# Optimization experiments

Measured on AMD Instinct MI355X. Metric: run time of the kernel, lower is better.

## Reference

```python
import jax, jax.numpy as jnp
import numpy as np

NEG = -1e9

def setup_inputs() -> dict:
    key = jax.random.key(0)
    ks = jax.random.split(key, 6)
    B, T, H = 32, 2048, 1024
    dec = jax.random.normal(ks[0], (B, H), dtype=jnp.float32)
    enc = jax.random.normal(ks[1], (B, T, H), dtype=jnp.float32)
    mask = jax.random.randint(ks[2], (B, T), 0, 2).astype(jnp.int32)
    scale = 1.0 / np.sqrt(H)
    W_enc = jax.random.normal(ks[3], (H, H), dtype=jnp.float32) * scale
    W_dec = jax.random.normal(ks[4], (H, H), dtype=jnp.float32) * scale
    v = jax.random.normal(ks[5], (H,), dtype=jnp.float32) * scale
    return {"decoder_hidden": dec, "encoder_outputs": enc, "mask": mask,
            "W_enc": W_enc, "W_dec": W_dec, "v": v}

def reference(decoder_hidden, encoder_outputs, mask, W_enc, W_dec, v):
    # enc proj: [B,T,H] @ W_enc^T ; dec proj: [B,H] @ W_dec^T broadcast over T
    enc_p = jnp.einsum('bth,oh->bto', encoder_outputs, W_enc)
    dec_p = jnp.einsum('bh,oh->bo', decoder_hidden, W_dec)[:, None, :]  # [B,1,H]
    energy = jnp.tanh(enc_p + dec_p)                                    # [B,T,H]
    scores = jnp.einsum('bth,h->bt', energy, v)                         # [B,T]
    scores = jnp.where(mask == 0, NEG, scores)
    attn_weights = jax.nn.softmax(scores, axis=1)                       # [B,T]
    context = jnp.einsum('bt,bth->bh', attn_weights, encoder_outputs)   # [B,H]
    return (context, attn_weights)
```

## Files before the change

### kernel.cpp

```cpp
#include <hip/hip_runtime.h>
#include <hip/hip_bf16.h>
#include <stdint.h>

#define B_ 32
#define T_ 2048
#define H_ 1024
#define M_ (B_*T_)

typedef __bf16 bf16x8 __attribute__((ext_vector_type(8)));
typedef float  f32x4  __attribute__((ext_vector_type(4)));
typedef float  f32x16 __attribute__((ext_vector_type(16)));

__device__ __forceinline__ float tanh_fast(float x) {
    float e = __expf(2.0f * x);
    return 1.0f - 2.0f / (e + 1.0f);
}

__device__ __forceinline__ bf16x8 cvt2(f32x4 f0, f32x4 f1) {
    bf16x8 h;
    h[0] = (__bf16)f0[0]; h[1] = (__bf16)f0[1]; h[2] = (__bf16)f0[2]; h[3] = (__bf16)f0[3];
    h[4] = (__bf16)f1[0]; h[5] = (__bf16)f1[1]; h[6] = (__bf16)f1[2]; h[7] = (__bf16)f1[3];
    return h;
}

__global__ __launch_bounds__(256) void k_prep(const float* __restrict__ We,
                                              __bf16* __restrict__ Wt,
                                              const float* __restrict__ dec,
                                              const float* __restrict__ Wd,
                                              float* __restrict__ decp) {
    int bx = blockIdx.x;
    int tid = threadIdx.x;
    if (bx < 512) {
        int tg = bx * 256 + tid;
        int lane = tg & 63;
        int c = (tg >> 6) & 31;
        int s = tg >> 11;
        int o = c * 32 + (lane & 31);
        int k = s * 16 + (lane >> 5) * 8;
        const f32x4* src = (const f32x4*)&We[(size_t)o * H_ + k];
        *(bf16x8*)&Wt[(size_t)tg * 8] = cvt2(src[0], src[1]);
    } else {
        int bxd = bx - 512;
        int b = bxd & 31, oc = bxd >> 5;
        int o = oc * 64 + (tid >> 2);
        int kq = tid & 3;
        const f32x4* wr = (const f32x4*)&Wd[(size_t)o * H_ + kq * 256];
        const f32x4* dr = (const f32x4*)&dec[(size_t)b * H_ + kq * 256];
        f32x4 s4 = {0.f, 0.f, 0.f, 0.f};
#pragma unroll 8
        for (int i = 0; i < 64; ++i) s4 += wr[i] * dr[i];
        float s = s4[0] + s4[1] + s4[2] + s4[3];
        s += __shfl_xor(s, 1);
        s += __shfl_xor(s, 2);
        if (kq == 0) decp[b * H_ + o] = s;
    }
}

__global__ __launch_bounds__(256, 2) void k_scores(const float* __restrict__ enc,
                                                   const float* __restrict__ decp,
                                                   const __bf16* __restrict__ Wt,
                                                   const float* __restrict__ v,
                                                   float* __restrict__ scores_p) {
    __shared__ __bf16 A_lds[2][64 * 32 * 8];
    __shared__ float red[4][64];

    const int tid = threadIdx.x;
    const int w = tid >> 6, lane = tid & 63;
    const int l5 = lane & 31, q2 = lane >> 5;

    const int bx = blockIdx.x;
    const int xs = bx & 7;
    const int q = bx >> 3;
    const int nt = q & 3;
    const int rg = (q >> 2) * 8 + xs;
    const int m0 = rg * 64;
    const int b = m0 >> 11;
    const int cg0 = nt * 8 + w * 2;

    float dp[2], vvv[2];
#pragma unroll
    for (int ct = 0; ct < 2; ++ct) {
        int col = (cg0 + ct) * 32 + l5;
        dp[ct]  = decp[b * H_ + col];
        vvv[ct] = v[col];
    }

    f32x16 acc[2][2];
#pragma unroll
    for (int rt = 0; rt < 2; ++rt)
#pragma unroll
        for (int ct = 0; ct < 2; ++ct)
#pragma unroll
            for (int g = 0; g < 16; ++g)
                acc[rt][ct][g] = dp[ct];

    const int ko_s = tid & 31;
    const int rbase = (tid >> 5) * 8;
    const float* sbase = &enc[(size_t)(m0 + rbase) * H_ + ko_s * 8];

    {
#pragma unroll
        for (int i = 0; i < 8; ++i) {
            const f32x4* s4 = (const f32x4*)(sbase + (size_t)i * H_);
            int row = rbase + i;
            int cell = row * 32 + ((ko_s & 24) | ((ko_s ^ row) & 7));
            *(bf16x8*)&A_lds[0][cell * 8] = cvt2(s4[0], s4[1]);
        }
    }
    __syncthreads();

    bf16x8 bb[4][2];
#pragma unroll
    for (int p = 0; p < 4; ++p)
#pragma unroll
        for (int ct = 0; ct < 2; ++ct)
            bb[p][ct] = *(const bf16x8*)&Wt[(((size_t)p * 32 + cg0 + ct) * 64 + lane) * 8];

#pragma unroll 1
    for (int kc = 0; kc < 4; ++kc) {
        const __bf16* buf = A_lds[kc & 1];

        f32x4 sr[8][2];
        if (kc < 3) {
            const float* sp0 = sbase + (size_t)(kc + 1) * 256;
#pragma unroll
            for (int i = 0; i < 8; ++i) {
                const f32x4* s4 = (const f32x4*)(sp0 + (size_t)i * H_);
                sr[i][0] = s4[0];
                sr[i][1] = s4[1];
            }
        }

        bf16x8 af[2][2];
#pragma unroll
        for (int p = 0; p < 2; ++p)
#pragma unroll
            for (int rt = 0; rt < 2; ++rt) {
                int row = rt * 32 + l5;
                int ko = p * 2 + q2;
                int cell = row * 32 + ((ko & 24) | ((ko ^ row) & 7));
                af[p][rt] = *(const bf16x8*)&buf[cell * 8];
            }

#pragma unroll
        for (int sl = 0; sl < 16; ++sl) {
            const int s = kc * 16 + sl;
            bf16x8 a0 = af[sl & 1][0], a1 = af[sl & 1][1];
            bf16x8 w0 = bb[s & 3][0],  w1 = bb[s & 3][1];

            {
                int sn = (s + 4) & 63;
#pragma unroll
                for (int ct = 0; ct < 2; ++ct)
                    bb[s & 3][ct] = *(const bf16x8*)&Wt[(((size_t)sn * 32 + cg0 + ct) * 64 + lane) * 8];
            }
            {
                int sl2 = (sl + 2) & 15;
#pragma unroll
                for (int rt = 0; rt < 2; ++rt) {
                    int row = rt * 32 + l5;
                    int ko = sl2 * 2 + q2;
                    int cell = row * 32 + ((ko & 24) | ((ko ^ row) & 7));
                    af[sl & 1][rt] = *(const bf16x8*)&buf[cell * 8];
                }
            }

            acc[0][0] = __builtin_amdgcn_mfma_f32_32x32x16_bf16(a0, w0, acc[0][0], 0, 0, 0);
            acc[0][1] = __builtin_amdgcn_mfma_f32_32x32x16_bf16(a0, w1, acc[0][1], 0, 0, 0);
            acc[1][0] = __builtin_amdgcn_mfma_f32_32x32x16_bf16(a1, w0, acc[1][0], 0, 0, 0);
            acc[1][1] = __builtin_amdgcn_mfma_f32_32x32x16_bf16(a1, w1, acc[1][1], 0, 0, 0);
        }

        if (kc < 3) {
            __bf16* dst = A_lds[(kc + 1) & 1];
#pragma unroll
            for (int i = 0; i < 8; ++i) {
                int row = rbase + i;
                int cell = row * 32 + ((ko_s & 24) | ((ko_s ^ row) & 7));
                *(bf16x8*)&dst[cell * 8] = cvt2(sr[i][0], sr[i][1]);
            }
        }
        __syncthreads();
    }

    float sp[2][16];
#pragma unroll
    for (int rt = 0; rt < 2; ++rt)
#pragma unroll
        for (int g = 0; g < 16; ++g)
            sp[rt][g] = tanh_fast(acc[rt][0][g]) * vvv[0] + tanh_fast(acc[rt][1][g]) * vvv[1];

#pragma unroll
    for (int rt = 0; rt < 2; ++rt)
#pragma unroll
        for (int g = 0; g < 16; ++g) {
            float s = sp[rt][g];
            s += __shfl_xor(s, 1);
            s += __shfl_xor(s, 2);
            s += __shfl_xor(s, 4);
            s += __shfl_xor(s, 8);
            s += __shfl_xor(s, 16);
            sp[rt][g] = s;
        }

    if (l5 == 0) {
#pragma unroll
        for (int rt = 0; rt < 2; ++rt)
#pragma unroll
            for (int g = 0; g < 16; ++g) {
                int row = rt * 32 + (g & 3) + 8 * (g >> 2) + 4 * q2;
                red[w][row] = sp[rt][g];
            }
    }
    __syncthreads();
    if (tid < 64) {
        float s = red[0][tid] + red[1][tid] + red[2][tid] + red[3][tid];
        scores_p[nt * M_ + m0 + tid] = s;
    }
}

__global__ __launch_bounds__(256) void k_softmax(const float* __restrict__ scores_p,
                                                 const int* __restrict__ mask,
                                                 float* __restrict__ attn) {
    int b = blockIdx.x;
    int tid = threadIdx.x;
    int w = tid >> 6, lane = tid & 63;
    __shared__ float sm[2][4];
    float val[8];
    float mx = -3e38f;
#pragma unroll
    for (int ii = 0; ii < 8; ++ii) {
        int idx = b * T_ + tid + ii * 256;
        float s = scores_p[idx] + scores_p[M_ + idx] + scores_p[2 * M_ + idx] + scores_p[3 * M_ + idx];
        s = (mask[idx] == 0) ? -1e9f : s;
        val[ii] = s;
        mx = fmaxf(mx, s);
    }
#pragma unroll
    for (int m = 1; m <= 32; m <<= 1) mx = fmaxf(mx, __shfl_xor(mx, m));
    if (lane == 0) sm[0][w] = mx;
    __syncthreads();
    mx = fmaxf(fmaxf(sm[0][0], sm[0][1]), fmaxf(sm[0][2], sm[0][3]));
    float lsum = 0.f;
#pragma unroll
    for (int ii = 0; ii < 8; ++ii) {
        val[ii] = __expf(val[ii] - mx);
        lsum += val[ii];
    }
#pragma unroll
    for (int m = 1; m <= 32; m <<= 1) lsum += __shfl_xor(lsum, m);
    if (lane == 0) sm[1][w] = lsum;
    __syncthreads();
    float inv = 1.0f / (sm[1][0] + sm[1][1] + sm[1][2] + sm[1][3]);
#pragma unroll
    for (int ii = 0; ii < 8; ++ii)
        attn[b * T_ + tid + ii * 256] = val[ii] * inv;
}

__global__ __launch_bounds__(512) void k_context(const float* __restrict__ enc,
                                                 const float* __restrict__ attn,
                                                 float* __restrict__ ctx) {
    __shared__ f32x4 cred[8][32];
    int bx = blockIdx.x;
    int b = bx >> 3, hc = bx & 7;
    int tid = threadIdx.x;
    int wv = tid >> 6, lane = tid & 63;
    int l5 = lane & 31, tq2 = lane >> 5;
    int h = hc * 128 + l5 * 4;
    const float* ap = &attn[b * T_ + wv * 256 + tq2];
    const float* ep = &enc[((size_t)b * T_ + wv * 256 + tq2) * H_ + h];
    f32x4 acc = {0.f, 0.f, 0.f, 0.f};
#pragma unroll 8
    for (int i = 0; i < 128; ++i) {
        float a = ap[2 * i];
        f32x4 e = *(const f32x4*)(ep + (size_t)2 * i * H_);
        acc += a * e;
    }
#pragma unroll
    for (int c = 0; c < 4; ++c) acc[c] += __shfl_xor(acc[c], 32);
    if (tq2 == 0) cred[wv][l5] = acc;
    __syncthreads();
    if (tid < 32) {
        f32x4 r = cred[0][tid];
#pragma unroll
        for (int j = 1; j < 8; ++j) r += cred[j][tid];
        *(f32x4*)&ctx[b * H_ + hc * 128 + tid * 4] = r;
    }
}

extern "C" void kernel_launch(void* const* d_in, const int* in_sizes, int n_in,
                              void* d_out, int out_size, void* d_ws, size_t ws_size,
                              hipStream_t stream) {
    (void)in_sizes; (void)n_in; (void)out_size; (void)ws_size;
    const float* dec  = (const float*)d_in[0];
    const float* enc  = (const float*)d_in[1];
    const int*   mask = (const int*)d_in[2];
    const float* We   = (const float*)d_in[3];
    const float* Wd   = (const float*)d_in[4];
    const float* v    = (const float*)d_in[5];

    float* out = (float*)d_out;
    char* ws = (char*)d_ws;
    float*  decp     = (float*)ws;
    float*  scores_p = (float*)(ws + 131072);
    __bf16* Wt       = (__bf16*)(ws + 131072 + 1048576);

    k_prep   <<<1024, 256, 0, stream>>>(We, Wt, dec, Wd, decp);
    k_scores <<<4096, 256, 0, stream>>>(enc, decp, Wt, v, scores_p);
    k_softmax<<<32, 256, 0, stream>>>(scores_p, mask, out + B_ * H_);
    k_context<<<256, 512, 0, stream>>>(enc, out + B_ * H_, out);
}
```

Baseline: 582.1 us.

## Pre-convert encoder to bf16 fragment layout and DMA it into LDS for scores GEMM

Adds a separate pass that converts the fp32 encoder outputs into a bf16 copy laid out in MFMA fragment order in workspace. The scores GEMM then streams that copy into LDS with global_load_lds DMA, using 128-row tiles and 8 waves per block. This removes the in-loop fp32-to-bf16 conversion and swizzled LDS stores from the GEMM, and doubles row reuse of the weight fragments. In exchange it adds an extra full read of the encoder plus a 128MB write and reread, and it needs a large workspace, falling back to the old kernel otherwise.

```diff
diff --git a/kernel.cpp b/kernel.cpp
--- a/kernel.cpp
+++ b/kernel.cpp
@@ -21,6 +21,12 @@
     h[0] = (__bf16)f0[0]; h[1] = (__bf16)f0[1]; h[2] = (__bf16)f0[2]; h[3] = (__bf16)f0[3];
     h[4] = (__bf16)f1[0]; h[5] = (__bf16)f1[1]; h[6] = (__bf16)f1[2]; h[7] = (__bf16)f1[3];
     return h;
+}
+
+__device__ __forceinline__ void dma16(const void* g, void* l) {
+    __builtin_amdgcn_global_load_lds(
+        (const __attribute__((address_space(1))) unsigned int*)g,
+        (__attribute__((address_space(3))) unsigned int*)l, 16, 0, 0);
 }
 
 __global__ __launch_bounds__(256) void k_prep(const float* __restrict__ We,
@@ -56,18 +62,170 @@
     }
 }
 
-__global__ __launch_bounds__(256, 2) void k_scores(const float* __restrict__ enc,
+__global__ __launch_bounds__(256) void k_conv(const float* __restrict__ enc,
+                                              __bf16* __restrict__ encT) {
+    __shared__ float Lf[128][132];
+    const int rg = blockIdx.x;
+    const int t = threadIdx.x;
+    const size_t rowbase = (size_t)rg * 128;
+#pragma unroll 1
+    for (int kc = 0; kc < 8; ++kc) {
+#pragma unroll
+        for (int i = 0; i < 16; ++i) {
+            int row = i * 8 + (t >> 5);
+            int qq = t & 31;
+            f32x4 val = *(const f32x4*)&enc[(rowbase + row) * H_ + kc * 128 + qq * 4];
+            *(f32x4*)&Lf[row][qq * 4] = val;
+        }
+        __syncthreads();
+#pragma unroll
+        for (int j = 0; j < 8; ++j) {
+            int cid = j * 256 + t;
+            int g = cid >> 6;
+            int lane = cid & 63;
+            int rt = g & 3, s = g >> 2;
+            int row = rt * 32 + (lane & 31);
+            int kl = s * 16 + (lane >> 5) * 8;
+            f32x4 f0 = *(const f32x4*)&Lf[row][kl];
+            f32x4 f1 = *(const f32x4*)&Lf[row][kl + 4];
+            *(bf16x8*)&encT[((((size_t)rg * 8 + kc) * 32 + g) * 64 + lane) * 8] = cvt2(f0, f1);
+        }
+        __syncthreads();
+    }
+}
+
+__global__ __launch_bounds__(512, 4) void k_scores(const __bf16* __restrict__ encT,
                                                    const float* __restrict__ decp,
                                                    const __bf16* __restrict__ Wt,
                                                    const float* __restrict__ v,
                                                    float* __restrict__ scores_p) {
-    __shared__ __bf16 A_lds[2][64 * 32 * 8];
-    __shared__ float red[4][64];
+    __shared__ __align__(16) __bf16 Abuf[2][32 * 64 * 8];
+    __shared__ float red[4][128];
 
     const int tid = threadIdx.x;
     const int w = tid >> 6, lane = tid & 63;
     const int l5 = lane & 31, q2 = lane >> 5;
-
+    const int wr = w >> 2, wc = w & 3;
+
+    const int bx = blockIdx.x;
+    const int xs = bx & 7;
+    const int q = bx >> 3;
+    const int ng = q & 3;
+    const int rg = (q >> 2) * 8 + xs;
+    const int m0 = rg * 128;
+    const int b = m0 >> 11;
+    const int c0 = ng * 8 + wc * 2;
+
+    f32x16 acc[2][2];
+#pragma unroll
+    for (int ct = 0; ct < 2; ++ct) {
+        float dpv = decp[b * H_ + (c0 + ct) * 32 + l5];
+#pragma unroll
+        for (int rr = 0; rr < 2; ++rr)
+#pragma unroll
+            for (int g = 0; g < 16; ++g)
+                acc[rr][ct][g] = dpv;
+    }
+
+    const size_t chunk0 = ((size_t)rg * 8) * 32 * 512;
+
+#pragma unroll
+    for (int i = 0; i < 4; ++i) {
+        int g = w * 4 + i;
+        dma16(&encT[chunk0 + (size_t)g * 512 + lane * 8], &Abuf[0][g * 512]);
+    }
+    __syncthreads();
+
+    bf16x8 b_cur[2], b_nxt[2];
+#pragma unroll
+    for (int ct = 0; ct < 2; ++ct)
+        b_cur[ct] = *(const bf16x8*)&Wt[(((size_t)0 * 32 + c0 + ct) * 64 + lane) * 8];
+
+#pragma unroll 1
+    for (int kc = 0; kc < 8; ++kc) {
+        if (kc < 7) {
+            const size_t cb = ((size_t)(rg * 8 + kc + 1)) * 32 * 512;
+#pragma unroll
+            for (int i = 0; i < 4; ++i) {
+                int g = w * 4 + i;
+                dma16(&encT[cb + (size_t)g * 512 + lane * 8], &Abuf[(kc + 1) & 1][g * 512]);
+            }
+        }
+        const __bf16* buf = Abuf[kc & 1];
+
+#pragma unroll
+        for (int sl = 0; sl < 8; ++sl) {
+            int sgn = (kc * 8 + sl + 1) & 63;
+#pragma unroll
+            for (int ct = 0; ct < 2; ++ct)
+                b_nxt[ct] = *(const bf16x8*)&Wt[(((size_t)sgn * 32 + c0 + ct) * 64 + lane) * 8];
+
+            bf16x8 af[2];
+#pragma unroll
+            for (int rr = 0; rr < 2; ++rr)
+                af[rr] = *(const bf16x8*)&buf[((sl * 4 + wr * 2 + rr) * 64 + lane) * 8];
+
+            acc[0][0] = __builtin_amdgcn_mfma_f32_32x32x16_bf16(af[0], b_cur[0], acc[0][0], 0, 0, 0);
+            acc[0][1] = __builtin_amdgcn_mfma_f32_32x32x16_bf16(af[0], b_cur[1], acc[0][1], 0, 0, 0);
+            acc[1][0] = __builtin_amdgcn_mfma_f32_32x32x16_bf16(af[1], b_cur[0], acc[1][0], 0, 0, 0);
+            acc[1][1] = __builtin_amdgcn_mfma_f32_32x32x16_bf16(af[1], b_cur[1], acc[1][1], 0, 0, 0);
+
+            b_cur[0] = b_nxt[0];
+            b_cur[1] = b_nxt[1];
+        }
+        __syncthreads();
+    }
+
+    float vv[2];
+#pragma unroll
+    for (int ct = 0; ct < 2; ++ct) vv[ct] = v[(c0 + ct) * 32 + l5];
+
+    float sp[2][16];
+#pragma unroll
+    for (int rr = 0; rr < 2; ++rr)
+#pragma unroll
+        for (int g = 0; g < 16; ++g)
+            sp[rr][g] = tanh_fast(acc[rr][0][g]) * vv[0] + tanh_fast(acc[rr][1][g]) * vv[1];
+
+#pragma unroll
+    for (int rr = 0; rr < 2; ++rr)
+#pragma unroll
+        for (int g = 0; g < 16; ++g) {
+            float s = sp[rr][g];
+            s += __shfl_xor(s, 1);
+            s += __shfl_xor(s, 2);
+            s += __shfl_xor(s, 4);
+            s += __shfl_xor(s, 8);
+            s += __shfl_xor(s, 16);
+            sp[rr][g] = s;
+        }
+
+    if (l5 == 0) {
+#pragma unroll
+        for (int rr = 0; rr < 2; ++rr)
+#pragma unroll
+            for (int g = 0; g < 16; ++g) {
+                int row = wr * 64 + rr * 32 + (g & 3) + 8 * (g >> 2) + 4 * q2;
+                red[wc][row] = sp[rr][g];
+            }
+    }
+    __syncthreads();
+    if (tid < 128) {
+        float s = red[0][tid] + red[1][tid] + red[2][tid] + red[3][tid];
+        scores_p[ng * M_ + m0 + tid] = s;
+    }
+}
+
+__global__ __launch_bounds__(256, 2) void k_scores_fb(const float* __restrict__ enc,
+                                                      const float* __restrict__ decp,
+                                                      const __bf16* __restrict__ Wt,
+                                                      const float* __restrict__ v,
+                                                      float* __restrict__ scores_p) {
+    __shared__ __bf16 A_lds[2][64 * 32 * 8];
+    __shared__ float red[4][64];
+    const int tid = threadIdx.x;
+    const int w = tid >> 6, lane = tid & 63;
+    const int l5 = lane & 31, q2 = lane >> 5;
     const int bx = blockIdx.x;
     const int xs = bx & 7;
     const int q = bx >> 3;
@@ -76,28 +234,23 @@
     const int m0 = rg * 64;
     const int b = m0 >> 11;
     const int cg0 = nt * 8 + w * 2;
-
     float dp[2], vvv[2];
 #pragma unroll
     for (int ct = 0; ct < 2; ++ct) {
         int col = (cg0 + ct) * 32 + l5;
-        dp[ct]  = decp[b * H_ + col];
+        dp[ct] = decp[b * H_ + col];
         vvv[ct] = v[col];
     }
-
     f32x16 acc[2][2];
 #pragma unroll
     for (int rt = 0; rt < 2; ++rt)
 #pragma unroll
         for (int ct = 0; ct < 2; ++ct)
 #pragma unroll
-            for (int g = 0; g < 16; ++g)
-                acc[rt][ct][g] = dp[ct];
-
+            for (int g = 0; g < 16; ++g) acc[rt][ct][g] = dp[ct];
     const int ko_s = tid & 31;
     const int rbase = (tid >> 5) * 8;
     const float* sbase = &enc[(size_t)(m0 + rbase) * H_ + ko_s * 8];
-
     {
 #pragma unroll
         for (int i = 0; i < 8; ++i) {
@@ -108,88 +261,55 @@
         }
     }
     __syncthreads();
-
-    bf16x8 bb[4][2];
-#pragma unroll
-    for (int p = 0; p < 4; ++p)
-#pragma unroll
-        for (int ct = 0; ct < 2; ++ct)
-            bb[p][ct] = *(const bf16x8*)&Wt[(((size_t)p * 32 + cg0 + ct) * 64 + lane) * 8];
-
+    bf16x8 b_cur[2];
+#pragma unroll
+    for (int ct = 0; ct < 2; ++ct)
+        b_cur[ct] = *(const bf16x8*)&Wt[(((size_t)0 * 32 + cg0 + ct) * 64 + lane) * 8];
 #pragma unroll 1
     for (int kc = 0; kc < 4; ++kc) {
         const __bf16* buf = A_lds[kc & 1];
-
-        f32x4 sr[8][2];
+#pragma unroll
+        for (int sl = 0; sl < 16; ++sl) {
+            const int s = kc * 16 + sl;
+            int sn = (s + 1) & 63;
+            bf16x8 b_nxt[2];
+#pragma unroll
+            for (int ct = 0; ct < 2; ++ct)
+                b_nxt[ct] = *(const bf16x8*)&Wt[(((size_t)sn * 32 + cg0 + ct) * 64 + lane) * 8];
+            bf16x8 af[2];
+#pragma unroll
+            for (int rt = 0; rt < 2; ++rt) {
+                int row = rt * 32 + l5;
+                int ko = sl * 2 + q2;
+                int cell = row * 32 + ((ko & 24) | ((ko ^ row) & 7));
+                af[rt] = *(const bf16x8*)&buf[cell * 8];
+            }
+            acc[0][0] = __builtin_amdgcn_mfma_f32_32x32x16_bf16(af[0], b_cur[0], acc[0][0], 0, 0, 0);
+            acc[0][1] = __builtin_amdgcn_mfma_f32_32x32x16_bf16(af[0], b_cur[1], acc[0][1], 0, 0, 0);
+            acc[1][0] = __builtin_amdgcn_mfma_f32_32x32x16_bf16(af[1], b_cur[0], acc[1][0], 0, 0, 0);
+            acc[1][1] = __builtin_amdgcn_mfma_f32_32x32x16_bf16(af[1], b_cur[1], acc[1][1], 0, 0, 0);
+            b_cur[0] = b_nxt[0];
+            b_cur[1] = b_nxt[1];
+        }
         if (kc < 3) {
+            __bf16* dst = A_lds[(kc + 1) & 1];
             const float* sp0 = sbase + (size_t)(kc + 1) * 256;
 #pragma unroll
             for (int i = 0; i < 8; ++i) {
                 const f32x4* s4 = (const f32x4*)(sp0 + (size_t)i * H_);
-                sr[i][0] = s4[0];
-                sr[i][1] = s4[1];
-            }
-        }
-
-        bf16x8 af[2][2];
-#pragma unroll
-        for (int p = 0; p < 2; ++p)
-#pragma unroll
-            for (int rt = 0; rt < 2; ++rt) {
-                int row = rt * 32 + l5;
-                int ko = p * 2 + q2;
-                int cell = row * 32 + ((ko & 24) | ((ko ^ row) & 7));
-                af[p][rt] = *(const bf16x8*)&buf[cell * 8];
-            }
-
-#pragma unroll
-        for (int sl = 0; sl < 16; ++sl) {
-            const int s = kc * 16 + sl;
-            bf16x8 a0 = af[sl & 1][0], a1 = af[sl & 1][1];
-            bf16x8 w0 = bb[s & 3][0],  w1 = bb[s & 3][1];
-
-            {
-                int sn = (s + 4) & 63;
-#pragma unroll
-                for (int ct = 0; ct < 2; ++ct)
-                    bb[s & 3][ct] = *(const bf16x8*)&Wt[(((size_t)sn * 32 + cg0 + ct) * 64 + lane) * 8];
-            }
-            {
-                int sl2 = (sl + 2) & 15;
-#pragma unroll
-                for (int rt = 0; rt < 2; ++rt) {
-                    int row = rt * 32 + l5;
-                    int ko = sl2 * 2 + q2;
-                    int cell = row * 32 + ((ko & 24) | ((ko ^ row) & 7));
-                    af[sl & 1][rt] = *(const bf16x8*)&buf[cell * 8];
-                }
-            }
-
-            acc[0][0] = __builtin_amdgcn_mfma_f32_32x32x16_bf16(a0, w0, acc[0][0], 0, 0, 0);
-            acc[0][1] = __builtin_amdgcn_mfma_f32_32x32x16_bf16(a0, w1, acc[0][1], 0, 0, 0);
-            acc[1][0] = __builtin_amdgcn_mfma_f32_32x32x16_bf16(a1, w0, acc[1][0], 0, 0, 0);
-            acc[1][1] = __builtin_amdgcn_mfma_f32_32x32x16_bf16(a1, w1, acc[1][1], 0, 0, 0);
-        }
-
-        if (kc < 3) {
-            __bf16* dst = A_lds[(kc + 1) & 1];
-#pragma unroll
-            for (int i = 0; i < 8; ++i) {
                 int row = rbase + i;
                 int cell = row * 32 + ((ko_s & 24) | ((ko_s ^ row) & 7));
-                *(bf16x8*)&dst[cell * 8] = cvt2(sr[i][0], sr[i][1]);
+                *(bf16x8*)&dst[cell * 8] = cvt2(s4[0], s4[1]);
             }
         }
         __syncthreads();
     }
-
     float sp[2][16];
 #pragma unroll
     for (int rt = 0; rt < 2; ++rt)
 #pragma unroll
         for (int g = 0; g < 16; ++g)
             sp[rt][g] = tanh_fast(acc[rt][0][g]) * vvv[0] + tanh_fast(acc[rt][1][g]) * vvv[1];
-
 #pragma unroll
     for (int rt = 0; rt < 2; ++rt)
 #pragma unroll
@@ -202,7 +322,6 @@
             s += __shfl_xor(s, 16);
             sp[rt][g] = s;
         }
-
     if (l5 == 0) {
 #pragma unroll
         for (int rt = 0; rt < 2; ++rt)
@@ -291,7 +410,7 @@
 extern "C" void kernel_launch(void* const* d_in, const int* in_sizes, int n_in,
                               void* d_out, int out_size, void* d_ws, size_t ws_size,
                               hipStream_t stream) {
-    (void)in_sizes; (void)n_in; (void)out_size; (void)ws_size;
+    (void)in_sizes; (void)n_in; (void)out_size;
     const float* dec  = (const float*)d_in[0];
     const float* enc  = (const float*)d_in[1];
     const int*   mask = (const int*)d_in[2];
@@ -304,9 +423,17 @@
     float*  decp     = (float*)ws;
     float*  scores_p = (float*)(ws + 131072);
     __bf16* Wt       = (__bf16*)(ws + 131072 + 1048576);
-
-    k_prep   <<<1024, 256, 0, stream>>>(We, Wt, dec, Wd, decp);
-    k_scores <<<4096, 256, 0, stream>>>(enc, decp, Wt, v, scores_p);
+    __bf16* encT     = (__bf16*)(ws + 3276800);
+
+    const size_t NEED = 3276800ull + (size_t)M_ * H_ * 2ull;
+
+    k_prep<<<1024, 256, 0, stream>>>(We, Wt, dec, Wd, decp);
+    if (ws_size >= NEED) {
+        k_conv  <<<512, 256, 0, stream>>>(enc, encT);
+        k_scores<<<2048, 512, 0, stream>>>(encT, decp, Wt, v, scores_p);
+    } else {
+        k_scores_fb<<<4096, 256, 0, stream>>>(enc, decp, Wt, v, scores_p);
+    }
     k_softmax<<<32, 256, 0, stream>>>(scores_p, mask, out + B_ * H_);
     k_context<<<256, 512, 0, stream>>>(enc, out + B_ * H_, out);
 }
```

After: 630.7 us. 8.3% more time.
